# Kernel optimization log

Measured on AMD Instinct MI355X. Metric: run time of the kernel, lower is better.

Reference implementation:

```python
import jax, jax.numpy as jnp
import numpy as np

TOP_K = 2


def setup_inputs() -> dict:
    key = jax.random.key(0)
    k0, k1, k2, k3 = jax.random.split(key, 4)
    B, T, C, E, D = 4, 2048, 1024, 8, 1024  # D = 4*C*top_k//E
    x = jax.random.normal(k0, (B, T, C), dtype=jnp.float32)
    s = 1.0 / np.sqrt(C)
    w_router = jax.random.normal(k1, (C, E), dtype=jnp.float32) * s
    w1 = jax.random.normal(k2, (E, C, D), dtype=jnp.float32) * s  # c_fc.weight.T per expert
    w2 = jax.random.normal(k3, (E, D, C), dtype=jnp.float32) * (1.0 / np.sqrt(D))  # c_proj.weight.T
    return {"x": x, "w_router": w_router, "w1": w1, "w2": w2}


def reference(x, w_router, w1, w2):
    B, T, C = x.shape
    xf = x.reshape(-1, C)  # [N, C]
    logits = xf @ w_router  # [N, E]
    top_vals, top_idx = jax.lax.top_k(logits, TOP_K)  # [N, k]
    probs = jax.nn.softmax(top_vals, axis=-1)  # softmax over selected experts only
    # Dense per-expert MLP (relu^2), identical math to per-token weight gather:
    h = jnp.square(jax.nn.relu(jnp.einsum('nc,ecd->ned', xf, w1)))  # [N, E, D]
    y_all = jnp.einsum('ned,edc->nec', h, w2)  # [N, E, C]
    y_sel = jnp.take_along_axis(y_all, top_idx[:, :, None], axis=1)  # [N, k, C]
    out = jnp.sum(y_sel * probs[:, :, None], axis=1)  # [N, C]
    return out.reshape(B, T, C)
```

## Files before the change

### kernel.cpp

```cpp
#include <hip/hip_runtime.h>
#include <stdint.h>

typedef unsigned short u16;
typedef unsigned int u32;

constexpr int C = 1024;
constexpr int E = 8;
constexpr int D = 1024;
constexpr int BM = 128, BN = 128, BK = 32;

typedef short s16x8 __attribute__((ext_vector_type(8)));
typedef float f32x4 __attribute__((ext_vector_type(4)));

__device__ __forceinline__ u16 f2bf(float f) {
  union { float f; u32 u; } v; v.f = f;
  return (u16)((v.u + 0x7FFFu + ((v.u >> 16) & 1u)) >> 16);
}
__device__ __forceinline__ float bf2f(u32 u) {
  union { u32 u; float f; } v; v.u = u << 16; return v.f;
}

typedef __attribute__((address_space(1))) const u32 gu32;
typedef __attribute__((address_space(3))) u32 lu32;
__device__ __forceinline__ void gl_lds16(const void* g, void* l) {
  __builtin_amdgcn_global_load_lds((gu32*)g, (lu32*)l, 16, 0, 0);
}
template <int N>
__device__ __forceinline__ void waitvm() {
  asm volatile("s_waitcnt vmcnt(%0)" :: "i"(N) : "memory");
  __builtin_amdgcn_sched_barrier(0);
}
__device__ __forceinline__ void bar() {
  __builtin_amdgcn_s_barrier();
  __builtin_amdgcn_sched_barrier(0);
}

__global__ void __launch_bounds__(256) k_wt(const float* __restrict__ w1,
                                            const float* __restrict__ w2,
                                            u16* __restrict__ w1t, u16* __restrict__ w2t,
                                            const float* __restrict__ wr,
                                            float* __restrict__ wrT,
                                            int* __restrict__ ints,
                                            const float* __restrict__ x,
                                            u16* __restrict__ xb, int Ntok) {
  int b = blockIdx.x;
  int t = threadIdx.x;
  if (b > 4096) {
    int xbid = b - 4097;
    const f32x4* src = (const f32x4*)x;
    uint2* dst = (uint2*)xb;
    int total = Ntok * (C / 4);
    for (int i = xbid * 256 + t; i < total; i += 1024 * 256) {
      f32x4 v = src[i];
      uint2 o;
      o.x = (u32)f2bf(v[0]) | ((u32)f2bf(v[1]) << 16);
      o.y = (u32)f2bf(v[2]) | ((u32)f2bf(v[3]) << 16);
      dst[i] = o;
    }
    return;
  }
  if (b == 4096) {
    if (t < 64) ints[t] = 0;
    for (int g = t; g < C * E; g += 256) wrT[(g & 7) * C + (g >> 3)] = wr[g];
    return;
  }
  __shared__ float tile[64][65];
  int which = b >> 11;
  int rem = b & 2047;
  int e = rem >> 8, kt = (rem >> 4) & 15, nt = rem & 15;
  const float* src = (which ? w2 : w1) + (size_t)e * C * D;
  u16* dst = (which ? w2t : w1t) + (size_t)e * C * D;
#pragma unroll
  for (int i = 0; i < 4; ++i) {
    int lin = i * 256 + t;
    int r = lin >> 4, c4 = lin & 15;
    f32x4 v = *(const f32x4*)(src + (size_t)(kt * 64 + r) * 1024 + nt * 64 + c4 * 4);
    tile[r][c4 * 4 + 0] = v[0]; tile[r][c4 * 4 + 1] = v[1];
    tile[r][c4 * 4 + 2] = v[2]; tile[r][c4 * 4 + 3] = v[3];
  }
  __syncthreads();
#pragma unroll
  for (int i = 0; i < 2; ++i) {
    int lin = i * 256 + t;
    int nr = lin >> 3, k8 = lin & 7;
    u32 o[4];
#pragma unroll
    for (int j = 0; j < 4; ++j)
      o[j] = (u32)f2bf(tile[k8 * 8 + 2 * j][nr]) |
             ((u32)f2bf(tile[k8 * 8 + 2 * j + 1][nr]) << 16);
    *(uint4*)(dst + (size_t)(nt * 64 + nr) * 1024 + kt * 64 + k8 * 8) = *(const uint4*)o;
  }
}

__global__ void __launch_bounds__(256) k_router(const float* __restrict__ x,
                                                const float* __restrict__ wrT,
                                                int* __restrict__ tok_e,
                                                float* __restrict__ tok_p,
                                                int* __restrict__ counts) {
  __shared__ float lg[32][9];
  __shared__ int cl[8];
  int t = threadIdx.x;
  int tok0 = blockIdx.x * 32;
  int tl = t >> 3, e = t & 7;
  if (t < 8) cl[t] = 0;
  size_t tok = (size_t)tok0 + tl;
  const f32x4* xr = (const f32x4*)(x + tok * C);
  const f32x4* wv4 = (const f32x4*)(wrT + e * C);
  float a0 = 0.f, a1 = 0.f, a2 = 0.f, a3 = 0.f;
#pragma unroll 4
  for (int i = 0; i < C / 4; ++i) {
    f32x4 xv = xr[i], wv = wv4[i];
    a0 += xv[0] * wv[0]; a1 += xv[1] * wv[1];
    a2 += xv[2] * wv[2]; a3 += xv[3] * wv[3];
  }
  lg[tl][e] = (a0 + a1) + (a2 + a3);
  __syncthreads();
  if (t < 32) {
    int myTok = tok0 + t;
    float v0 = -1e30f; int i0 = 0;
#pragma unroll
    for (int q = 0; q < 8; ++q) { float v = lg[t][q]; if (v > v0) { v0 = v; i0 = q; } }
    float v1 = -1e30f; int i1 = 0;
#pragma unroll
    for (int q = 0; q < 8; ++q) {
      if (q == i0) continue;
      float v = lg[t][q]; if (v > v1) { v1 = v; i1 = q; }
    }
    float dd = expf(v1 - v0);
    float s = 1.f / (1.f + dd);
    tok_e[myTok * 2 + 0] = i0; tok_e[myTok * 2 + 1] = i1;
    tok_p[myTok * 2 + 0] = s;  tok_p[myTok * 2 + 1] = dd * s;
    atomicAdd(&cl[i0], 1); atomicAdd(&cl[i1], 1);
  }
  __syncthreads();
  if (t < 8 && cl[t] > 0) atomicAdd(&counts[t], cl[t]);
}

__global__ void __launch_bounds__(256) k_build(const int* __restrict__ tok_e,
                                               const int* __restrict__ counts,
                                               int* __restrict__ cnt2,
                                               int* __restrict__ offs,
                                               int* __restrict__ list_tok,
                                               int* __restrict__ inv) {
  int gid = blockIdx.x * 256 + threadIdx.x;
  int offv[9]; int off = 0;
#pragma unroll
  for (int q = 0; q < 8; ++q) { offv[q] = off; off += (counts[q] + (BM - 1)) & ~(BM - 1); }
  offv[8] = off;
  if (blockIdx.x == 0 && threadIdx.x < 9) offs[threadIdx.x] = offv[threadIdx.x];
  int lane = threadIdx.x & 63;
#pragma unroll
  for (int s = 0; s < 2; ++s) {
    int e = tok_e[gid * 2 + s];
    for (int q = 0; q < 8; ++q) {
      unsigned long long mask = __ballot(e == q);
      if (mask == 0ull) continue;
      int leader = __ffsll(mask) - 1;
      int cnt = __popcll(mask);
      int base = 0;
      if (lane == leader) base = atomicAdd(&cnt2[q], cnt);
      base = __shfl(base, leader, 64);
      if (e == q) {
        int pos = offv[q] + base + __popcll(mask & ((1ull << lane) - 1ull));
        list_tok[pos] = gid;
        inv[gid * 2 + s] = pos;
      }
    }
  }
}

template <int MODE>
__global__ void __launch_bounds__(256, 3) k_gemm(const u16* __restrict__ A,
                                                 const u16* __restrict__ Bt,
                                                 u16* __restrict__ Hout,
                                                 const int* __restrict__ list_tok,
                                                 const int* __restrict__ offs,
                                                 int Ntok) {
  __shared__ u16 A0[BM * BK], B0[BN * BK], A1[BM * BK], B1[BN * BK], A2[BM * BK], B2[BN * BK];
  int b = blockIdx.x;
  int nper = gridDim.x >> 3;
  int logical = (b & 7) * nper + (b >> 3);
  int m0 = (logical >> 3) * BM;
  int n0 = (logical & 7) * BN;
  if (m0 >= offs[8]) return;
  int e = 0;
#pragma unroll
  for (int q = 1; q < 8; ++q) e += (m0 >= offs[q]);

  int t = threadIdx.x;
  int l = t & 63, w = t >> 6;
  int wm = w >> 1, wn = w & 1;

  const u16* ag[2]; const u16* bg[2];
#pragma unroll
  for (int j = 0; j < 2; ++j) {
    int row = w * 32 + j * 16 + (l >> 2);
    int coff = (((l & 3) ^ ((row >> 1) & 3)) << 3);
    if (MODE == 0) {
      int tk = list_tok[m0 + row];
      tk = (tk < 0 || tk >= Ntok) ? 0 : tk;
      ag[j] = A + (size_t)tk * C + coff;
    } else {
      ag[j] = A + (size_t)(m0 + row) * C + coff;
    }
    bg[j] = Bt + (size_t)e * C * D + (size_t)(n0 + row) * 1024 + coff;
  }
  u16* a0 = &A0[w * 1024]; u16* b0 = &B0[w * 1024];
  u16* a1 = &A1[w * 1024]; u16* b1 = &B1[w * 1024];
  u16* a2 = &A2[w * 1024]; u16* b2 = &B2[w * 1024];

  f32x4 acc[4][4];
#pragma unroll
  for (int m = 0; m < 4; ++m)
#pragma unroll
    for (int n = 0; n < 4; ++n) acc[m][n] = (f32x4){0.f, 0.f, 0.f, 0.f};

  auto STAGE = [&](int k0, u16* al, u16* bl) {
#pragma unroll
    for (int j = 0; j < 2; ++j) {
      gl_lds16(ag[j] + k0, al + j * 512);
      gl_lds16(bg[j] + k0, bl + j * 512);
    }
  };
  auto COMPUTE = [&](const u16* Al, const u16* Bl) {
    s16x8 af[4], bf[4];
    int cr = l >> 4;
#pragma unroll
    for (int m = 0; m < 4; ++m) {
      int row = wm * 64 + m * 16 + (l & 15);
      af[m] = *(const s16x8*)&Al[row * BK + ((cr ^ ((row >> 1) & 3)) << 3)];
    }
#pragma unroll
    for (int n = 0; n < 4; ++n) {
      int row = wn * 64 + n * 16 + (l & 15);
      bf[n] = *(const s16x8*)&Bl[row * BK + ((cr ^ ((row >> 1) & 3)) << 3)];
    }
    __builtin_amdgcn_s_setprio(1);
#pragma unroll
    for (int m = 0; m < 4; ++m)
#pragma unroll
      for (int n = 0; n < 4; ++n)
        acc[m][n] = __builtin_amdgcn_mfma_f32_16x16x32_bf16(af[m], bf[n], acc[m][n], 0, 0, 0);
    __builtin_amdgcn_s_setprio(0);
  };

  STAGE(0, a0, b0);
  STAGE(BK, a1, b1);
#pragma unroll 1
  for (int tt = 0; tt < 30; tt += 3) {
    STAGE((tt + 2) * BK, a2, b2); waitvm<8>(); bar(); COMPUTE(A0, B0); bar();
    STAGE((tt + 3) * BK, a0, b0); waitvm<8>(); bar(); COMPUTE(A1, B1); bar();
    STAGE((tt + 4) * BK, a1, b1); waitvm<8>(); bar(); COMPUTE(A2, B2); bar();
  }
  waitvm<4>(); bar(); COMPUTE(A0, B0);
  waitvm<0>(); bar(); COMPUTE(A1, B1);

#pragma unroll
  for (int m = 0; m < 4; ++m) {
#pragma unroll
    for (int r = 0; r < 4; ++r) {
      int grow = m0 + wm * 64 + m * 16 + ((l >> 4) << 2) + r;
      u16* hp = Hout + (size_t)grow * 1024 + n0 + wn * 64 + (l & 15);
#pragma unroll
      for (int n = 0; n < 4; ++n) {
        float v = acc[m][n][r];
        if (MODE == 0) { v = fmaxf(v, 0.f); v = v * v; }
        hp[n * 16] = f2bf(v);
      }
    }
  }
}

__global__ void __launch_bounds__(256) k_combine(const u16* __restrict__ Y,
                                                 const int* __restrict__ inv,
                                                 const float* __restrict__ tok_p,
                                                 float* __restrict__ out) {
  int gid = blockIdx.x * 4 + (threadIdx.x >> 6);
  int l = threadIdx.x & 63;
  int s0 = inv[gid * 2 + 0], s1 = inv[gid * 2 + 1];
  float p0 = tok_p[gid * 2 + 0], p1 = tok_p[gid * 2 + 1];
  const uint4* y0 = (const uint4*)(Y + (size_t)s0 * 1024);
  const uint4* y1 = (const uint4*)(Y + (size_t)s1 * 1024);
  f32x4* o = (f32x4*)(out + (size_t)gid * 1024);
#pragma unroll
  for (int i = 0; i < 2; ++i) {
    int c = i * 64 + l;
    uint4 a = y0[c], bb = y1[c];
    f32x4 r0, r1;
    r0[0] = p0 * bf2f(a.x & 0xffffu) + p1 * bf2f(bb.x & 0xffffu);
    r0[1] = p0 * bf2f(a.x >> 16)     + p1 * bf2f(bb.x >> 16);
    r0[2] = p0 * bf2f(a.y & 0xffffu) + p1 * bf2f(bb.y & 0xffffu);
    r0[3] = p0 * bf2f(a.y >> 16)     + p1 * bf2f(bb.y >> 16);
    r1[0] = p0 * bf2f(a.z & 0xffffu) + p1 * bf2f(bb.z & 0xffffu);
    r1[1] = p0 * bf2f(a.z >> 16)     + p1 * bf2f(bb.z >> 16);
    r1[2] = p0 * bf2f(a.w & 0xffffu) + p1 * bf2f(bb.w & 0xffffu);
    r1[3] = p0 * bf2f(a.w >> 16)     + p1 * bf2f(bb.w >> 16);
    o[c * 2 + 0] = r0;
    o[c * 2 + 1] = r1;
  }
}

extern "C" void kernel_launch(void* const* d_in, const int* in_sizes, int n_in,
                              void* d_out, int out_size, void* d_ws, size_t ws_size,
                              hipStream_t stream) {
  const float* x  = (const float*)d_in[0];
  const float* wr = (const float*)d_in[1];
  const float* w1 = (const float*)d_in[2];
  const float* w2 = (const float*)d_in[3];
  float* out = (float*)d_out;
  const int Ntok = in_sizes[0] / C;
  const int ROWS = 2 * Ntok + E * BM;

  char* p = (char*)d_ws;
  u16* xb  = (u16*)p; p += (size_t)Ntok * C * 2;
  u16* w1t = (u16*)p; p += (size_t)E * C * D * 2;
  u16* w2t = (u16*)p; p += (size_t)E * C * D * 2;
  u16* h   = (u16*)p; p += (size_t)ROWS * D * 2;
  u16* y   = (u16*)p; p += (size_t)ROWS * C * 2;
  float* wrT = (float*)p; p += (size_t)C * E * 4;
  int* list_tok = (int*)p; p += (size_t)ROWS * 4;
  int* inv = (int*)p; p += (size_t)Ntok * 2 * 4;
  int* tok_e = (int*)p; p += (size_t)Ntok * 2 * 4;
  float* tok_p = (float*)p; p += (size_t)Ntok * 2 * 4;
  int* ints = (int*)p; p += 256;
  int* counts = ints;
  int* offs = ints + 16;
  int* cnt2 = ints + 32;
  (void)ws_size; (void)n_in; (void)out_size;

  k_wt<<<4097 + 1024, 256, 0, stream>>>(w1, w2, w1t, w2t, wr, wrT, ints, x, xb, Ntok);
  k_router<<<Ntok / 32, 256, 0, stream>>>(x, wrT, tok_e, tok_p, counts);
  k_build<<<Ntok / 256, 256, 0, stream>>>(tok_e, counts, cnt2, offs, list_tok, inv);
  k_gemm<0><<<(ROWS / BM) * 8, 256, 0, stream>>>(xb, w1t, h, list_tok, offs, Ntok);
  k_gemm<1><<<(ROWS / BM) * 8, 256, 0, stream>>>(h, w2t, y, list_tok, offs, Ntok);
  k_combine<<<Ntok / 4, 256, 0, stream>>>(y, inv, tok_p, out);
}
```

Baseline: 202.1 us.

## Load A tiles directly from global into registers, keep only B in LDS

The A operand (gathered token rows) is no longer staged through shared memory. Each lane loads its MFMA A fragments straight from global memory into a triple-buffered register set, while B keeps the LDS async pipeline. This halves LDS usage and drops the LDS reads for A. The cost is higher register pressure (12 extra vector registers of A fragments per stage set), possibly hurting occupancy at launch bounds of 3. It also duplicates A global loads across the two wn waves, and the per-lane loads are less coalesced.

```diff
diff --git a/kernel.cpp b/kernel.cpp
--- a/kernel.cpp
+++ b/kernel.cpp
@@ -176,7 +176,7 @@
                                                  const int* __restrict__ list_tok,
                                                  const int* __restrict__ offs,
                                                  int Ntok) {
-  __shared__ u16 A0[BM * BK], B0[BN * BK], A1[BM * BK], B1[BN * BK], A2[BM * BK], B2[BN * BK];
+  __shared__ u16 B0[BN * BK], B1[BN * BK], B2[BN * BK];
   int b = blockIdx.x;
   int nper = gridDim.x >> 3;
   int logical = (b & 7) * nper + (b >> 3);
@@ -191,23 +191,27 @@
   int l = t & 63, w = t >> 6;
   int wm = w >> 1, wn = w & 1;
 
-  const u16* ag[2]; const u16* bg[2];
+  const u16* bg[2];
 #pragma unroll
   for (int j = 0; j < 2; ++j) {
     int row = w * 32 + j * 16 + (l >> 2);
     int coff = (((l & 3) ^ ((row >> 1) & 3)) << 3);
+    bg[j] = Bt + (size_t)e * C * D + (size_t)(n0 + row) * 1024 + coff;
+  }
+  u16* b0 = &B0[w * 1024]; u16* b1 = &B1[w * 1024]; u16* b2 = &B2[w * 1024];
+
+  const u16* ap[4];
+#pragma unroll
+  for (int m = 0; m < 4; ++m) {
+    int rowl = wm * 64 + m * 16 + (l & 15);
     if (MODE == 0) {
-      int tk = list_tok[m0 + row];
+      int tk = list_tok[m0 + rowl];
       tk = (tk < 0 || tk >= Ntok) ? 0 : tk;
-      ag[j] = A + (size_t)tk * C + coff;
+      ap[m] = A + (size_t)tk * C + ((l >> 4) << 3);
     } else {
-      ag[j] = A + (size_t)(m0 + row) * C + coff;
-    }
-    bg[j] = Bt + (size_t)e * C * D + (size_t)(n0 + row) * 1024 + coff;
-  }
-  u16* a0 = &A0[w * 1024]; u16* b0 = &B0[w * 1024];
-  u16* a1 = &A1[w * 1024]; u16* b1 = &B1[w * 1024];
-  u16* a2 = &A2[w * 1024]; u16* b2 = &B2[w * 1024];
+      ap[m] = A + (size_t)(m0 + rowl) * C + ((l >> 4) << 3);
+    }
+  }
 
   f32x4 acc[4][4];
 #pragma unroll
@@ -215,21 +219,19 @@
 #pragma unroll
     for (int n = 0; n < 4; ++n) acc[m][n] = (f32x4){0.f, 0.f, 0.f, 0.f};
 
-  auto STAGE = [&](int k0, u16* al, u16* bl) {
-#pragma unroll
-    for (int j = 0; j < 2; ++j) {
-      gl_lds16(ag[j] + k0, al + j * 512);
-      gl_lds16(bg[j] + k0, bl + j * 512);
-    }
+  s16x8 a0r[4], a1r[4], a2r[4];
+
+  auto STAGEB = [&](int k0, u16* bl) {
+#pragma unroll
+    for (int j = 0; j < 2; ++j) gl_lds16(bg[j] + k0, bl + j * 512);
   };
-  auto COMPUTE = [&](const u16* Al, const u16* Bl) {
-    s16x8 af[4], bf[4];
+  auto LOADA = [&](int k0, s16x8* ar) {
+#pragma unroll
+    for (int m = 0; m < 4; ++m) ar[m] = *(const s16x8*)(ap[m] + k0);
+  };
+  auto COMPUTE = [&](const s16x8* ar, const u16* Bl) {
+    s16x8 bf[4];
     int cr = l >> 4;
-#pragma unroll
-    for (int m = 0; m < 4; ++m) {
-      int row = wm * 64 + m * 16 + (l & 15);
-      af[m] = *(const s16x8*)&Al[row * BK + ((cr ^ ((row >> 1) & 3)) << 3)];
-    }
 #pragma unroll
     for (int n = 0; n < 4; ++n) {
       int row = wn * 64 + n * 16 + (l & 15);
@@ -240,20 +242,20 @@
     for (int m = 0; m < 4; ++m)
 #pragma unroll
       for (int n = 0; n < 4; ++n)
-        acc[m][n] = __builtin_amdgcn_mfma_f32_16x16x32_bf16(af[m], bf[n], acc[m][n], 0, 0, 0);
+        acc[m][n] = __builtin_amdgcn_mfma_f32_16x16x32_bf16(ar[m], bf[n], acc[m][n], 0, 0, 0);
     __builtin_amdgcn_s_setprio(0);
   };
 
-  STAGE(0, a0, b0);
-  STAGE(BK, a1, b1);
+  STAGEB(0, b0);  LOADA(0, a0r);
+  STAGEB(BK, b1); LOADA(BK, a1r);
 #pragma unroll 1
   for (int tt = 0; tt < 30; tt += 3) {
-    STAGE((tt + 2) * BK, a2, b2); waitvm<8>(); bar(); COMPUTE(A0, B0); bar();
-    STAGE((tt + 3) * BK, a0, b0); waitvm<8>(); bar(); COMPUTE(A1, B1); bar();
-    STAGE((tt + 4) * BK, a1, b1); waitvm<8>(); bar(); COMPUTE(A2, B2); bar();
-  }
-  waitvm<4>(); bar(); COMPUTE(A0, B0);
-  waitvm<0>(); bar(); COMPUTE(A1, B1);
+    STAGEB((tt + 2) * BK, b2); LOADA((tt + 2) * BK, a2r); waitvm<12>(); bar(); COMPUTE(a0r, B0); bar();
+    STAGEB((tt + 3) * BK, b0); LOADA((tt + 3) * BK, a0r); waitvm<12>(); bar(); COMPUTE(a1r, B1); bar();
+    STAGEB((tt + 4) * BK, b1); LOADA((tt + 4) * BK, a1r); waitvm<12>(); bar(); COMPUTE(a2r, B2); bar();
+  }
+  waitvm<6>(); bar(); COMPUTE(a0r, B0);
+  waitvm<0>(); bar(); COMPUTE(a1r, B1);
 
 #pragma unroll
   for (int m = 0; m < 4; ++m) {
```

Result: slower. 284.7 us (+40.9%).
